# Performance work log

Measured on AMD Instinct MI355X. Metric: run time of the kernel, lower is better.

Reference implementation:

```python
import jax, jax.numpy as jnp
import numpy as np

N = 100000          # nodes
F_IN = 500          # num_features
HID = 256           # hidden
C = 40              # out_classes
E = 2302585         # ~ N*ln(N)*ec, doubled (both directions) in spar_samp
ALPHA0 = 0.1        # att[0][0] = alpha*(1-alpha)**0


def setup_inputs() -> dict:
    key = jax.random.key(0)
    ks = jax.random.split(key, 8)
    x = jax.random.normal(ks[0], (N, F_IN), dtype=jnp.float32)
    W1 = jax.random.normal(ks[1], (F_IN, HID), dtype=jnp.float32) * (1.0 / np.sqrt(F_IN))
    b1 = jnp.zeros((HID,), dtype=jnp.float32)
    W2 = jax.random.normal(ks[2], (HID, C), dtype=jnp.float32) * (1.0 / np.sqrt(HID))
    b2 = jnp.zeros((C,), dtype=jnp.float32)
    edge_row = jax.random.randint(ks[3], (E,), 0, N, dtype=jnp.int64) if jax.config.jax_enable_x64 else jax.random.randint(ks[3], (E,), 0, N, dtype=jnp.int32)
    edge_col = jax.random.randint(ks[4], (E,), 0, N, dtype=edge_row.dtype)
    # sampled importance weights: deg^{-1/2}*deg^{-1/2}*(M/num_edgess) -> small positive floats
    edge_val = jax.random.uniform(ks[5], (E,), dtype=jnp.float32, minval=0.001, maxval=0.05)
    return {"x": x, "W1": W1, "b1": b1, "W2": W2, "b2": b2,
            "edge_row": edge_row, "edge_col": edge_col, "edge_val": edge_val}


def reference(x, W1, b1, W2, b2, edge_row, edge_col, edge_val):
    # eval mode: dropout is identity
    h = jax.nn.relu(x @ W1 + b1)          # [N, HID]
    h = h @ W2 + b2                       # [N, C]
    # sparse propagation: out[r] += val * h[c]  (scatter-add SpMM)
    msg = edge_val[:, None] * h[edge_col]            # [E, C] gather
    agg = jax.ops.segment_sum(msg, edge_row, num_segments=N)  # [N, C]
    out = h * ALPHA0 + agg
    return jax.nn.log_softmax(out, axis=1)
```

## Files before the change

kernel.cpp:

```cpp
#include <hip/hip_runtime.h>
#include <hip/hip_bf16.h>


#define N_NODES 100000
#define F_IN    500
#define HID     256
#define C_OUT   40
#define ALPHA0  0.1f
#define H2STRIDE 64

#define RPB     64
#define NBUCK   ((N_NODES + RPB - 1) / RPB)
#define NCH     1024
#define SCAN_M  (NBUCK * NCH)
#define SCAN_CHUNK 2048
#define NBS     ((SCAN_M + SCAN_CHUNK - 1) / SCAN_CHUNK)
#define BCAPL   1792

typedef short short8 __attribute__((ext_vector_type(8)));
typedef float f32x4  __attribute__((ext_vector_type(4)));

__device__ __forceinline__ short f2bf(float f) {
  union { float f; unsigned u; } x; x.f = f;
  unsigned r = x.u + 0x7fffu + ((x.u >> 16) & 1u);
  return (short)(r >> 16);
}
__device__ __forceinline__ float bf2f(short s) {
  union { unsigned u; float f; } x; x.u = ((unsigned)(unsigned short)s) << 16;
  return x.f;
}
__device__ __forceinline__ unsigned cvtpk(float lo, float hi) {
  unsigned r;
  asm("v_cvt_pk_bf16_f32 %0, %1, %2" : "=v"(r) : "v"(lo), "v"(hi));
  return r;
}
__device__ __forceinline__ void lbar() {
  asm volatile("s_waitcnt lgkmcnt(0)" ::: "memory");
  __builtin_amdgcn_s_barrier();
}
__device__ __forceinline__ void gll16(const float* g, const char* l) {
  __builtin_amdgcn_global_load_lds(
      (const __attribute__((address_space(1))) void*)g,
      (__attribute__((address_space(3))) void*)l, 16, 0, 0);
}

__global__ __launch_bounds__(256) void k_pack_weights(
    const float* __restrict__ W1, const float* __restrict__ W2,
    short* __restrict__ W1S, short* __restrict__ W2T)
{
  int i = blockIdx.x * 256 + threadIdx.x;
  if (i < 16*256*32) {
    int kc  = i >> 13;
    int idx = i & 8191;
    int n   = idx >> 5;
    int kk  = idx & 31;
    int k   = kc*32 + kk;
    float v = (k < F_IN) ? W1[k*HID + n] : 0.f;
    W1S[i] = f2bf(v);
  } else {
    int j = i - 16*256*32;
    if (j < 48*256) {
      int n = j >> 8;
      int k = j & 255;
      float v = (n < C_OUT) ? W2[k*C_OUT + n] : 0.f;
      W2T[j] = f2bf(v);
    }
  }
}

__global__ __launch_bounds__(512, 4) void k_fused_mlp(
    const float* __restrict__ x, const float* __restrict__ b1v,
    const float* __restrict__ b2v,
    const short* __restrict__ W1S, const short* __restrict__ W2T,
    short* __restrict__ h2b)
{
  __shared__ __align__(16) char smem[65536];
  short (*Hl)[256] = (short(*)[256])smem;

  const int tid  = threadIdx.x;
  const int w    = tid >> 6;
  const int lane = tid & 63;
  const int lr   = lane & 15;
  const int quad = lane >> 4;
  const int wr   = w >> 2;
  const int wc   = w & 3;
  const int row0 = blockIdx.x * 128;

  const int s_rl0 = (w*2)*8 + (lane>>3);
  const int s_rl1 = (w*2+1)*8 + (lane>>3);
  const int ksw   = ((lane&7) ^ ((lane>>3)&7)) * 4;
  const float* gp0 = x + (size_t)min(row0 + s_rl0, N_NODES-1) * F_IN;
  const float* gp1 = x + (size_t)min(row0 + s_rl1, N_NODES-1) * F_IN;
  const char* l0 = smem + (w*2)*1024;
  const char* l1 = smem + (w*2+1)*1024;

  f32x4 acc[4][4] = {};

  #pragma unroll
  for (int p = 0; p < 2; ++p) {
    int kb = p*32 + ksw;
    const float* a0 = (kb + 4 <= F_IN) ? gp0 + kb : x;
    const float* a1 = (kb + 4 <= F_IN) ? gp1 + kb : x;
    gll16(a0, l0 + p*16384);
    gll16(a1, l1 + p*16384);
  }

  const short* bbase = W1S + (wc*64 + lr)*32 + quad*8;
  const int m2 = lr & 7;

  #pragma unroll
  for (int kc = 0; kc < 16; ++kc) {
    short8 bf4[4];
    #pragma unroll
    for (int t = 0; t < 4; ++t)
      bf4[t] = *(const short8*)(bbase + kc*8192 + t*16*32);
    __builtin_amdgcn_sched_barrier(0);

    if (kc < 14) {
      int kb = (kc+2)*32 + ksw;
      const float* a0 = (kb + 4 <= F_IN) ? gp0 + kb : x;
      const float* a1 = (kb + 4 <= F_IN) ? gp1 + kb : x;
      gll16(a0, l0 + ((kc+2)&3)*16384);
      gll16(a1, l1 + ((kc+2)&3)*16384);
      __builtin_amdgcn_sched_barrier(0);
      asm volatile("s_waitcnt vmcnt(8)" ::: "memory");
    } else if (kc == 14) {
      asm volatile("s_waitcnt vmcnt(6)" ::: "memory");
    } else {
      asm volatile("s_waitcnt vmcnt(4)" ::: "memory");
    }
    __builtin_amdgcn_s_barrier();

    const char* Abase = smem + (kc & 3)*16384;
    short8 af[4];
    #pragma unroll
    for (int t = 0; t < 4; ++t) {
      int rl = wr*64 + t*16 + lr;
      f32x4 u0 = *(const f32x4*)(Abase + rl*128 + (((quad*2  ) ^ m2) << 4));
      f32x4 u1 = *(const f32x4*)(Abase + rl*128 + (((quad*2+1) ^ m2) << 4));
      union { unsigned u[4]; short8 s; } pk;
      pk.u[0] = cvtpk(u0[0], u0[1]);
      pk.u[1] = cvtpk(u0[2], u0[3]);
      pk.u[2] = cvtpk(u1[0], u1[1]);
      pk.u[3] = cvtpk(u1[2], u1[3]);
      af[t] = pk.s;
    }

    #pragma unroll
    for (int rt = 0; rt < 4; ++rt)
      #pragma unroll
      for (int ct = 0; ct < 4; ++ct)
        acc[rt][ct] = __builtin_amdgcn_mfma_f32_16x16x32_bf16(af[rt], bf4[ct], acc[rt][ct], 0, 0, 0);
  }
  lbar();

  #pragma unroll
  for (int ct = 0; ct < 4; ++ct) {
    int col = wc*64 + ct*16 + lr;
    int cg = col >> 3, ci = col & 7;
    float bias = b1v[col];
    #pragma unroll
    for (int rt = 0; rt < 4; ++rt) {
      #pragma unroll
      for (int r = 0; r < 4; ++r) {
        int row = wr*64 + rt*16 + quad*4 + r;
        float v = fmaxf(acc[rt][ct][r] + bias, 0.f);
        Hl[row][((cg ^ (row & 31)) << 3) | ci] = f2bf(v);
      }
    }
  }
  lbar();

  f32x4 acc2[3] = {};
  const int arow = w*16 + lr;
  #pragma unroll
  for (int kc2 = 0; kc2 < 8; ++kc2) {
    int gg = kc2*4 + quad;
    short8 a2 = *(const short8*)&Hl[arow][(gg ^ (arow & 31)) << 3];
    #pragma unroll
    for (int nt = 0; nt < 3; ++nt) {
      short8 b2 = *(const short8*)(W2T + (nt*16 + lr)*256 + kc2*32 + quad*8);
      acc2[nt] = __builtin_amdgcn_mfma_f32_16x16x32_bf16(a2, b2, acc2[nt], 0, 0, 0);
    }
  }

  #pragma unroll
  for (int nt = 0; nt < 3; ++nt) {
    int col = nt*16 + lr;
    float bias = (col < C_OUT) ? b2v[col] : 0.f;
    #pragma unroll
    for (int r = 0; r < 4; ++r) {
      int row = row0 + w*16 + quad*4 + r;
      if (row < N_NODES) {
        float v = (col < C_OUT) ? (acc2[nt][r] + bias) : 0.f;
        h2b[(long)row * H2STRIDE + col] = f2bf(v);
      }
    }
  }
  {
    int col = 48 + lr;
    #pragma unroll
    for (int r = 0; r < 4; ++r) {
      int row = row0 + w*16 + quad*4 + r;
      if (row < N_NODES) h2b[(long)row * H2STRIDE + col] = 0;
    }
  }
}

__global__ __launch_bounds__(256) void k_hist2(
    const int* __restrict__ erow, int* __restrict__ offs, int E, int CH)
{
  __shared__ int h[NBUCK];
  int tid = threadIdx.x, c = blockIdx.x;
  for (int b = tid; b < NBUCK; b += 256) h[b] = 0;
  __syncthreads();
  int e0 = c * CH, e1 = min(E, e0 + CH);
  if (e0 < e1) {
    int g0 = e0 >> 2, g1 = e1 >> 2;
    const int4* rp = (const int4*)erow;
    for (int g = g0 + tid; g < g1; g += 256) {
      int4 r4 = rp[g];
      atomicAdd(&h[r4.x >> 6], 1);
      atomicAdd(&h[r4.y >> 6], 1);
      atomicAdd(&h[r4.z >> 6], 1);
      atomicAdd(&h[r4.w >> 6], 1);
    }
    for (int e = (g1 << 2) + tid; e < e1; e += 256)
      atomicAdd(&h[erow[e] >> 6], 1);
  }
  __syncthreads();
  for (int b = tid; b < NBUCK; b += 256) offs[b * NCH + c] = h[b];
}

__global__ __launch_bounds__(256) void k_scan1(
    int* __restrict__ offs, int* __restrict__ bsums)
{
  __shared__ int sh[256];
  int tid = threadIdx.x;
  int base = blockIdx.x * SCAN_CHUNK + tid * 8;
  int d[8];
  #pragma unroll
  for (int k = 0; k < 8; ++k)
    d[k] = (base + k < SCAN_M) ? offs[base + k] : 0;
  int s = 0;
  #pragma unroll
  for (int k = 0; k < 8; ++k) s += d[k];
  sh[tid] = s;
  __syncthreads();
  for (int o = 1; o < 256; o <<= 1) {
    int v = (tid >= o) ? sh[tid - o] : 0;
    __syncthreads();
    if (tid >= o) sh[tid] += v;
    __syncthreads();
  }
  int run = sh[tid] - s;
  #pragma unroll
  for (int k = 0; k < 8; ++k) {
    if (base + k < SCAN_M) offs[base + k] = run;
    run += d[k];
  }
  if (tid == 255) bsums[blockIdx.x] = sh[255];
}

__global__ __launch_bounds__(256) void k_scan2(int* __restrict__ bsums) {
  __shared__ int sh[256];
  int tid = threadIdx.x;
  int d[4];
  int s = 0;
  #pragma unroll
  for (int k = 0; k < 4; ++k) {
    int i = tid * 4 + k;
    d[k] = (i < NBS) ? bsums[i] : 0;
    s += d[k];
  }
  sh[tid] = s;
  __syncthreads();
  for (int o = 1; o < 256; o <<= 1) {
    int u = (tid >= o) ? sh[tid - o] : 0;
    __syncthreads();
    if (tid >= o) sh[tid] += u;
    __syncthreads();
  }
  int run = sh[tid] - s;
  #pragma unroll
  for (int k = 0; k < 4; ++k) {
    int i = tid * 4 + k;
    if (i < NBS) bsums[i] = run;
    run += d[k];
  }
}

__global__ __launch_bounds__(256) void k_split(
    const int* __restrict__ erow, const int* __restrict__ ecol,
    const float* __restrict__ eval, const int* __restrict__ offs,
    const int* __restrict__ bsums, int2* __restrict__ sorted,
    int* __restrict__ bstart, int E, int CH)
{
  __shared__ int cur[NBUCK];
  int tid = threadIdx.x, c = blockIdx.x;

  for (int b = tid; b < NBUCK; b += 256) {
    int m = b * NCH + c;
    int val = offs[m] + bsums[m >> 11];
    cur[b] = val;
    if (c == 0) bstart[b] = val;
  }
  if (c == 0 && tid == 0) bstart[NBUCK] = E;
  __syncthreads();

  int e0 = c * CH, e1 = min(E, e0 + CH);
  if (e0 >= e1) return;
  int g0 = e0 >> 2, g1 = e1 >> 2;
  const int4*   rp = (const int4*)erow;
  const int4*   cp = (const int4*)ecol;
  const float4* vp = (const float4*)eval;
  for (int g = g0 + tid; g < g1; g += 256) {
    int4 r4 = rp[g];
    int4 c4 = cp[g];
    float4 v4 = vp[g];
    int p0 = atomicAdd(&cur[r4.x >> 6], 1);
    int p1 = atomicAdd(&cur[r4.y >> 6], 1);
    int p2 = atomicAdd(&cur[r4.z >> 6], 1);
    int p3 = atomicAdd(&cur[r4.w >> 6], 1);
    int2 cv;
    cv.x = c4.x | ((r4.x & 63) << 17); cv.y = __float_as_int(v4.x); sorted[p0] = cv;
    cv.x = c4.y | ((r4.y & 63) << 17); cv.y = __float_as_int(v4.y); sorted[p1] = cv;
    cv.x = c4.z | ((r4.z & 63) << 17); cv.y = __float_as_int(v4.z); sorted[p2] = cv;
    cv.x = c4.w | ((r4.w & 63) << 17); cv.y = __float_as_int(v4.w); sorted[p3] = cv;
  }
  for (int e = (g1 << 2) + tid; e < e1; e += 256) {
    int r = erow[e];
    int pos = atomicAdd(&cur[r >> 6], 1);
    int2 cv;
    cv.x = ecol[e] | ((r & 63) << 17);
    cv.y = __float_as_int(eval[e]);
    sorted[pos] = cv;
  }
}

__global__ __launch_bounds__(256) void k_csr_spmm(
    const int* __restrict__ bstart, const int2* __restrict__ sorted,
    const short* __restrict__ h2b, float* __restrict__ out)
{
  __shared__ int2 eS[BCAPL];
  __shared__ int h[RPB];
  __shared__ int roff[RPB];
  __shared__ int cur[RPB];
  int tid = threadIdx.x, b = blockIdx.x;
  int lane = tid & 63, w = tid >> 6;
  int start = bstart[b], end = bstart[b + 1];
  int cnt = end - start;

  int2 cv[7];
  int nloc = 0;
  for (int i = tid, k = 0; i < cnt; i += 256, ++k) { cv[k] = sorted[start + i]; nloc = k + 1; }

  if (tid < RPB) h[tid] = 0;
  __syncthreads();
  for (int k = 0; k < nloc; ++k)
    atomicAdd(&h[((unsigned)cv[k].x) >> 17], 1);
  __syncthreads();
  if (tid < RPB) roff[tid] = h[tid];
  __syncthreads();
  for (int o = 1; o < RPB; o <<= 1) {
    int u = (tid >= o && tid < RPB) ? roff[tid - o] : 0;
    __syncthreads();
    if (tid >= o && tid < RPB) roff[tid] += u;
    __syncthreads();
  }
  if (tid < RPB) cur[tid] = roff[tid] - h[tid];
  __syncthreads();
  for (int k = 0; k < nloc; ++k) {
    unsigned rl = ((unsigned)cv[k].x) >> 17;
    int p = atomicAdd(&cur[rl], 1);
    if (p < BCAPL) eS[p] = cv[k];
  }
  __syncthreads();

  for (int rr = 0; rr < 16; ++rr) {
    int r = w * 16 + rr;
    int row = b * RPB + r;
    if (row >= N_NODES) continue;
    float acc = ALPHA0 * bf2f(h2b[(size_t)row * H2STRIDE + lane]);
    int e  = roff[r] - h[r];
    int ee = roff[r];
    for (; e + 7 < ee; e += 8) {
      int2 cc[8];
      float gg[8];
      #pragma unroll
      for (int j = 0; j < 8; ++j) cc[j] = eS[e + j];
      #pragma unroll
      for (int j = 0; j < 8; ++j)
        gg[j] = bf2f(h2b[(size_t)(cc[j].x & 0x1FFFF) * H2STRIDE + lane]);
      #pragma unroll
      for (int j = 0; j < 8; ++j) acc += __int_as_float(cc[j].y) * gg[j];
    }
    for (; e + 3 < ee; e += 4) {
      int2 c0 = eS[e], c1 = eS[e+1], c2 = eS[e+2], c3 = eS[e+3];
      float g0 = bf2f(h2b[(size_t)(c0.x & 0x1FFFF) * H2STRIDE + lane]);
      float g1 = bf2f(h2b[(size_t)(c1.x & 0x1FFFF) * H2STRIDE + lane]);
      float g2 = bf2f(h2b[(size_t)(c2.x & 0x1FFFF) * H2STRIDE + lane]);
      float g3 = bf2f(h2b[(size_t)(c3.x & 0x1FFFF) * H2STRIDE + lane]);
      acc += __int_as_float(c0.y) * g0;
      acc += __int_as_float(c1.y) * g1;
      acc += __int_as_float(c2.y) * g2;
      acc += __int_as_float(c3.y) * g3;
    }
    for (; e < ee; ++e) {
      int2 c0 = eS[e];
      acc += __int_as_float(c0.y) * bf2f(h2b[(size_t)(c0.x & 0x1FFFF) * H2STRIDE + lane]);
    }
    float m = (lane < C_OUT) ? acc : -INFINITY;
    #pragma unroll
    for (int o = 32; o > 0; o >>= 1) m = fmaxf(m, __shfl_xor(m, o));
    float ev = (lane < C_OUT) ? __expf(acc - m) : 0.f;
    float s = ev;
    #pragma unroll
    for (int o = 32; o > 0; o >>= 1) s += __shfl_xor(s, o);
    if (lane < C_OUT) out[(long)row * C_OUT + lane] = acc - m - __logf(s);
  }
}

extern "C" void kernel_launch(void* const* d_in, const int* in_sizes, int n_in,
                              void* d_out, int out_size, void* d_ws, size_t ws_size,
                              hipStream_t stream) {
  const float* x    = (const float*)d_in[0];
  const float* W1   = (const float*)d_in[1];
  const float* b1   = (const float*)d_in[2];
  const float* W2   = (const float*)d_in[3];
  const float* b2   = (const float*)d_in[4];
  const int*   erow = (const int*)d_in[5];
  const int*   ecol = (const int*)d_in[6];
  const float* eval = (const float*)d_in[7];
  const int E  = in_sizes[5];
  int CH = (E + NCH - 1) / NCH;
  CH = (CH + 3) & ~3;

  char* p = (char*)d_ws;
  short* h2b    = (short*)p;  p += (size_t)N_NODES * H2STRIDE * 2;
  short* W1S    = (short*)p;  p += (size_t)16*256*32 * 2;
  short* W2T    = (short*)p;  p += (size_t)48*256 * 2;
  int*   offs   = (int*)p;    p += (size_t)SCAN_M * 4;
  int*   bsums  = (int*)p;    p += 1024 * 4;
  int*   bstart = (int*)p;    p += (size_t)(NBUCK + 4) * 4;
  int2*  sorted = (int2*)p;
  float* out = (float*)d_out;

  k_pack_weights<<<(16*256*32 + 48*256 + 255)/256, 256, 0, stream>>>(W1, W2, W1S, W2T);
  k_fused_mlp<<<(N_NODES + 127)/128, 512, 0, stream>>>(x, b1, b2, W1S, W2T, h2b);
  k_hist2<<<NCH, 256, 0, stream>>>(erow, offs, E, CH);
  k_scan1<<<NBS, 256, 0, stream>>>(offs, bsums);
  k_scan2<<<1, 256, 0, stream>>>(bsums);
  k_split<<<NCH, 256, 0, stream>>>(erow, ecol, eval, offs, bsums, sorted, bstart, E, CH);
  k_csr_spmm<<<NBUCK, 256, 0, stream>>>(bstart, sorted, h2b, out);
}
```

Baseline: 505.6 us.

## Fuse edge-row histogram into MLP kernel tail and add transpose pass

The per-chunk bucket histogram of edge rows now runs at the end of the fused MLP kernel, reusing its shared memory, with each MLP block taking chunks grid-stride. Counts are written chunk-major with coalesced stores, and a new tiled transpose kernel converts them to the bucket-major layout the scan expects. The aim is to drop a separate launch and overlap the histogram's memory-bound work with MLP blocks, at the cost of an extra transpose pass and a scratch buffer. It also lengthens the MLP kernel's tail.

After: 502.3 us. About the same (-0.7%).

```diff
diff --git a/kernel.cpp b/kernel.cpp
--- a/kernel.cpp
+++ b/kernel.cpp
@@ -11,6 +11,7 @@
 
 #define RPB     64
 #define NBUCK   ((N_NODES + RPB - 1) / RPB)
+#define NBUCKP  1568
 #define NCH     1024
 #define SCAN_M  (NBUCK * NCH)
 #define SCAN_CHUNK 2048
@@ -72,7 +73,8 @@
     const float* __restrict__ x, const float* __restrict__ b1v,
     const float* __restrict__ b2v,
     const short* __restrict__ W1S, const short* __restrict__ W2T,
-    short* __restrict__ h2b)
+    short* __restrict__ h2b,
+    const int* __restrict__ erow, int* __restrict__ hs, int E, int CH)
 {
   __shared__ __align__(16) char smem[65536];
   short (*Hl)[256] = (short(*)[256])smem;
@@ -205,31 +207,54 @@
       if (row < N_NODES) h2b[(long)row * H2STRIDE + col] = 0;
     }
   }
-}
-
-__global__ __launch_bounds__(256) void k_hist2(
-    const int* __restrict__ erow, int* __restrict__ offs, int E, int CH)
-{
-  __shared__ int h[NBUCK];
-  int tid = threadIdx.x, c = blockIdx.x;
-  for (int b = tid; b < NBUCK; b += 256) h[b] = 0;
-  __syncthreads();
-  int e0 = c * CH, e1 = min(E, e0 + CH);
-  if (e0 < e1) {
-    int g0 = e0 >> 2, g1 = e1 >> 2;
-    const int4* rp = (const int4*)erow;
-    for (int g = g0 + tid; g < g1; g += 256) {
-      int4 r4 = rp[g];
-      atomicAdd(&h[r4.x >> 6], 1);
-      atomicAdd(&h[r4.y >> 6], 1);
-      atomicAdd(&h[r4.z >> 6], 1);
-      atomicAdd(&h[r4.w >> 6], 1);
-    }
-    for (int e = (g1 << 2) + tid; e < e1; e += 256)
-      atomicAdd(&h[erow[e] >> 6], 1);
-  }
-  __syncthreads();
-  for (int b = tid; b < NBUCK; b += 256) offs[b * NCH + c] = h[b];
+
+  int* hcnt = (int*)smem;
+  for (int cc = blockIdx.x; cc < NCH; cc += gridDim.x) {
+    lbar();
+    for (int b = tid; b < NBUCK; b += 512) hcnt[b] = 0;
+    __syncthreads();
+    int e0 = cc * CH, e1 = min(E, e0 + CH);
+    if (e0 < e1) {
+      int g0 = e0 >> 2, g1 = e1 >> 2;
+      const int4* rp = (const int4*)erow;
+      for (int g = g0 + tid; g < g1; g += 512) {
+        int4 r4 = rp[g];
+        atomicAdd(&hcnt[r4.x >> 6], 1);
+        atomicAdd(&hcnt[r4.y >> 6], 1);
+        atomicAdd(&hcnt[r4.z >> 6], 1);
+        atomicAdd(&hcnt[r4.w >> 6], 1);
+      }
+      for (int e = (g1 << 2) + tid; e < e1; e += 512)
+        atomicAdd(&hcnt[erow[e] >> 6], 1);
+    }
+    __syncthreads();
+    for (int b = tid; b < NBUCK; b += 512)
+      hs[(size_t)cc * NBUCKP + b] = hcnt[b];
+  }
+}
+
+__global__ __launch_bounds__(256) void k_transpose(
+    const int* __restrict__ hs, int* __restrict__ offs)
+{
+  __shared__ int t[64][65];
+  int cb = blockIdx.x & 15;
+  int bb = blockIdx.x >> 4;
+  int c0 = cb * 64, b0 = bb * 64;
+  int j  = threadIdx.x & 63;
+  int i0 = threadIdx.x >> 6;
+  #pragma unroll
+  for (int k = 0; k < 16; ++k) {
+    int i = i0 + k * 4;
+    int b = b0 + j;
+    t[i][j] = (b < NBUCK) ? hs[(size_t)(c0 + i) * NBUCKP + b] : 0;
+  }
+  __syncthreads();
+  #pragma unroll
+  for (int k = 0; k < 16; ++k) {
+    int i = i0 + k * 4;
+    int b = b0 + i;
+    if (b < NBUCK) offs[(size_t)b * NCH + c0 + j] = t[j][i];
+  }
 }
 
 __global__ __launch_bounds__(256) void k_scan1(
@@ -440,6 +465,7 @@
   short* h2b    = (short*)p;  p += (size_t)N_NODES * H2STRIDE * 2;
   short* W1S    = (short*)p;  p += (size_t)16*256*32 * 2;
   short* W2T    = (short*)p;  p += (size_t)48*256 * 2;
+  int*   hs     = (int*)p;    p += (size_t)NCH * NBUCKP * 4;
   int*   offs   = (int*)p;    p += (size_t)SCAN_M * 4;
   int*   bsums  = (int*)p;    p += 1024 * 4;
   int*   bstart = (int*)p;    p += (size_t)(NBUCK + 4) * 4;
@@ -447,8 +473,9 @@
   float* out = (float*)d_out;
 
   k_pack_weights<<<(16*256*32 + 48*256 + 255)/256, 256, 0, stream>>>(W1, W2, W1S, W2T);
-  k_fused_mlp<<<(N_NODES + 127)/128, 512, 0, stream>>>(x, b1, b2, W1S, W2T, h2b);
-  k_hist2<<<NCH, 256, 0, stream>>>(erow, offs, E, CH);
+  k_fused_mlp<<<(N_NODES + 127)/128, 512, 0, stream>>>(x, b1, b2, W1S, W2T, h2b,
+                                                       erow, hs, E, CH);
+  k_transpose<<<16 * 25, 256, 0, stream>>>(hs, offs);
   k_scan1<<<NBS, 256, 0, stream>>>(offs, bsums);
   k_scan2<<<1, 256, 0, stream>>>(bsums);
   k_split<<<NCH, 256, 0, stream>>>(erow, ecol, eval, offs, bsums, sorted, bstart, E, CH);
```
